# Optimization experiments

Measured on AMD Instinct MI355X. Metric: run time of the kernel, lower is better.

The kernel has to match this reference:

```python
import jax, jax.numpy as jnp
from jax import lax
import numpy as np

B, C_IN, IMG = 128, 3, 64
NH, D, K = 128, 256, 1024
BETA = 0.1        # beta buffer initialized to beta_start
BA_ITERS = 5
EPS = 1e-10


def _conv(x, w, b, stride, pad):
    y = lax.conv_general_dilated(x, w, (stride, stride), ((pad, pad), (pad, pad)),
                                 dimension_numbers=("NCHW", "OIHW", "NCHW"))
    return y + b[None, :, None, None]


def _convT(x, w, b):
    # PyTorch ConvTranspose2d(k=4, s=2, p=1); w: [Cin, Cout, 4, 4]
    wt = jnp.flip(w, (2, 3)).transpose(1, 0, 2, 3)  # -> [Cout, Cin, 4, 4]
    y = lax.conv_general_dilated(x, wt, (1, 1), ((2, 2), (2, 2)),
                                 lhs_dilation=(2, 2),
                                 dimension_numbers=("NCHW", "OIHW", "NCHW"))
    return y + b[None, :, None, None]


def _res(x, w1, b1, w2, b2):
    h = jax.nn.relu(_conv(x, w1, b1, 1, 1))
    h = _conv(h, w2, b2, 1, 1)
    return jax.nn.relu(h + x)


def setup_inputs() -> dict:
    key = jax.random.key(0)
    ks = iter(jax.random.split(key, 40))

    def w(shape):
        fan_in = int(np.prod(shape[1:]))
        return jax.random.normal(next(ks), shape, jnp.float32) / np.float32(np.sqrt(fan_in))

    z = lambda n: jnp.zeros((n,), jnp.float32)
    inp = {"x": jax.random.normal(next(ks), (B, C_IN, IMG, IMG), jnp.float32)}
    inp.update(
        ew1=w((NH, 3, 4, 4)), eb1=z(NH),
        ew2=w((2 * NH, NH, 4, 4)), eb2=z(2 * NH),
        ew3=w((D, 2 * NH, 3, 3)), eb3=z(D),
        er1aw=w((D, D, 3, 3)), er1ab=z(D), er1bw=w((D, D, 3, 3)), er1bb=z(D),
        er2aw=w((D, D, 3, 3)), er2ab=z(D), er2bw=w((D, D, 3, 3)), er2bb=z(D),
        codebook=jax.random.uniform(next(ks), (K, D), jnp.float32, -1.0 / K, 1.0 / K),
        pi=jnp.full((K,), 1.0 / K, jnp.float32),
        dr1aw=w((D, D, 3, 3)), dr1ab=z(D), dr1bw=w((D, D, 3, 3)), dr1bb=z(D),
        dr2aw=w((D, D, 3, 3)), dr2ab=z(D), dr2bw=w((D, D, 3, 3)), dr2bb=z(D),
        dw1=w((2 * NH, D, 3, 3)), db1=z(2 * NH),
        dwt2=w((2 * NH, NH, 4, 4)), dbt2=z(NH),
        dwt3=w((NH, 3, 4, 4)), dbt3=z(3),
    )
    return inp


def reference(x, ew1, eb1, ew2, eb2, ew3, eb3,
              er1aw, er1ab, er1bw, er1bb, er2aw, er2ab, er2bw, er2bb,
              codebook, pi,
              dr1aw, dr1ab, dr1bw, dr1bb, dr2aw, dr2ab, dr2bw, dr2bb,
              dw1, db1, dwt2, dbt2, dwt3, dbt3):
    # ---- encoder: [B,3,H,W] -> [B,D,H/4,W/4] ----
    h = jax.nn.relu(_conv(x, ew1, eb1, 2, 1))
    h = jax.nn.relu(_conv(h, ew2, eb2, 2, 1))
    h = jax.nn.relu(_conv(h, ew3, eb3, 1, 1))
    h = _res(h, er1aw, er1ab, er1bw, er1bb)
    z = _res(h, er2aw, er2ab, er2bw, er2bb)

    Bn, Dn, Hl, Wl = z.shape
    zf = z.transpose(0, 2, 3, 1).reshape(-1, Dn)  # [N, D]

    # squared euclidean distances [N, K]
    d = (jnp.sum(zf * zf, axis=1, keepdims=True)
         + jnp.sum(codebook * codebook, axis=1)
         - 2.0 * (zf @ codebook.T))

    # ---- Blahut-Arimoto iterations ----
    Q = pi
    for _ in range(BA_ITERS):
        logits = jnp.log(jnp.clip(Q, EPS)) - BETA * d  # [N, K]
        P = jax.nn.softmax(logits, axis=1)
        Q = jnp.clip(jnp.mean(P, axis=0), EPS)

    zq_soft = P @ codebook                              # [N, D]
    idx = jnp.argmax(P, axis=1)

    commit = 0.25 * jnp.mean((zf - lax.stop_gradient(zq_soft)) ** 2)
    cb_loss = jnp.mean((zq_soft - lax.stop_gradient(zf)) ** 2)
    ent = -jnp.sum(Q * jnp.log(jnp.clip(Q, EPS)))
    ent_loss = -0.01 * ent

    zq_hard = codebook[idx]
    zq = zq_soft + lax.stop_gradient(zq_hard - zq_soft)  # straight-through
    zq = zq.reshape(Bn, Hl, Wl, Dn).transpose(0, 3, 1, 2)

    # ---- decoder ----
    h = _res(zq, dr1aw, dr1ab, dr1bw, dr1bb)
    h = _res(h, dr2aw, dr2ab, dr2bw, dr2bb)
    h = jax.nn.relu(_conv(h, dw1, db1, 1, 1))
    h = jax.nn.relu(_convT(h, dwt2, dbt2))
    x_recon = _convT(h, dwt3, dbt3)
    return x_recon, commit, cb_loss, ent_loss
```

## Files before the change

kernel.cpp:

```cpp
#include <hip/hip_runtime.h>
#include <math.h>

#define NB   128
#define DC   256
#define SP   256
#define NROW 32768
#define KCB  1024
#define BETA_F 0.1f
#define EPSQ 1e-10f

typedef __attribute__((ext_vector_type(8))) short s16x8;
typedef __attribute__((ext_vector_type(4))) short s16x4;
typedef __attribute__((ext_vector_type(4))) float f32x4;

__device__ __forceinline__ short f2bf(float f) {
  unsigned u = __builtin_bit_cast(unsigned, f);
  unsigned r = (u + 0x7FFFu + ((u >> 16) & 1u)) >> 16;
  return (short)r;
}
__device__ __forceinline__ float bf2f(short s) {
  unsigned u = ((unsigned)(unsigned short)s) << 16;
  return __builtin_bit_cast(float, u);
}
__device__ __forceinline__ unsigned pack2(float a, float b) {
  return (unsigned)(unsigned short)f2bf(a) | ((unsigned)(unsigned short)f2bf(b) << 16);
}

__global__ void init0_kernel(short* __restrict__ zerob)
{
  if (threadIdx.x < 8) zerob[threadIdx.x] = 0;
}

__global__ void w3t10_kernel(
    const float* __restrict__ w0, const float* __restrict__ w1,
    const float* __restrict__ w2, const float* __restrict__ w3,
    const float* __restrict__ w4, const float* __restrict__ w5,
    const float* __restrict__ w6, const float* __restrict__ w7,
    const float* __restrict__ w8, const float* __restrict__ w9,
    short* __restrict__ o)
{
  const float* ws[10] = {w0, w1, w2, w3, w4, w5, w6, w7, w8, w9};
  const float* w = ws[blockIdx.y];
  const int i = blockIdx.x * 256 + threadIdx.x;
  const int ci = i & 255, co = (i >> 8) & 255, j = i >> 16;
  o[(size_t)blockIdx.y * 589824 + i] = f2bf(w[((size_t)(co * 256 + ci)) * 9 + j]);
}
__global__ void w2t_kernel(const float* __restrict__ w, short* __restrict__ o)
{
  const int i = blockIdx.x * 256 + threadIdx.x;
  const int ci = i & 127, co = (i >> 7) & 255, j = i >> 15;
  o[i] = f2bf(w[((size_t)(co * 128 + ci)) * 16 + j]);
}
__global__ void wtt2_kernel(const float* __restrict__ w, short* __restrict__ o)
{
  const int i = blockIdx.x * 256 + threadIdx.x;
  const int ci = i & 255, co = (i >> 8) & 127, j = (i >> 15) & 3, p = i >> 17;
  const int po = p >> 1, pq = p & 1, a = j >> 1, b2 = j & 1;
  const int kh = (1 - po) + 2 * a, kw = (1 - pq) + 2 * b2;
  o[i] = f2bf(w[((size_t)(ci * 128 + co)) * 16 + kh * 4 + kw]);
}
__global__ void cbbf_kernel(const float* __restrict__ cb, short* __restrict__ o)
{
  const int i = blockIdx.x * 256 + threadIdx.x;
  o[i] = f2bf(cb[i]);
}
__global__ void cbt_kernel(const float* __restrict__ cb, short* __restrict__ o)
{
  const int i = blockIdx.x * 256 + threadIdx.x;
  const int d = i >> 10, k = i & 1023;
  o[i] = f2bf(cb[(size_t)k * 256 + d]);
}

__global__ __launch_bounds__(256) void conv1_kernel(
    const float* __restrict__ x, const float* __restrict__ w,
    const float* __restrict__ bias, short* __restrict__ out)
{
  __shared__ float li[3][34][34];
  const int tid = threadIdx.x;
  const int tile = blockIdx.x;
  const int b = blockIdx.y;
  const int qy = tile >> 1, qx = tile & 1;
  const int ihlo = qy * 32 - 1, iwlo = qx * 32 - 1;
  for (int ci = 0; ci < 3; ++ci)
    for (int s = tid; s < 1156; s += 256) {
      const int r = s / 34, c = s - r * 34;
      const int ih = ihlo + r, iw = iwlo + c;
      float v = 0.f;
      if ((unsigned)ih < 64u && (unsigned)iw < 64u)
        v = x[((size_t)(b * 3 + ci) * 64 + ih) * 64 + iw];
      li[ci][r][c] = v;
    }
  __syncthreads();

  const int wv = tid >> 6, l = tid & 63;
  const int co0 = 2 * l, co1 = 2 * l + 1;
  float w0[48], w1[48];
#pragma unroll
  for (int j = 0; j < 48; ++j) {
    w0[j] = w[(size_t)co0 * 48 + j];
    w1[j] = w[(size_t)co1 * 48 + j];
  }
  const float b0 = bias[co0], b1 = bias[co1];

  for (int pass = 0; pass < 64; ++pass) {
    const int pix = pass * 4 + wv;
    const int py = pix >> 4, px = pix & 15;
    float s0 = b0, s1 = b1;
#pragma unroll
    for (int ci = 0; ci < 3; ++ci)
#pragma unroll
      for (int kh = 0; kh < 4; ++kh)
#pragma unroll
        for (int kw = 0; kw < 4; ++kw) {
          const int j = ci * 16 + kh * 4 + kw;
          const float v = li[ci][2 * py + kh][2 * px + kw];
          s0 = fmaf(v, w0[j], s0);
          s1 = fmaf(v, w1[j], s1);
        }
    s0 = fmaxf(s0, 0.f);
    s1 = fmaxf(s1, 0.f);
    const int oh = qy * 16 + py, ow = qx * 16 + px;
    ((unsigned*)(out + ((size_t)b * 1024 + oh * 32 + ow) * 128))[l] = pack2(s0, s1);
  }
}

template<int MODE, int KIT, int AK, int KPN, int TS>
__global__ __launch_bounds__(256) void igemm_kernel(
    const short* __restrict__ Abuf, const short* __restrict__ Bw,
    const float* __restrict__ bias, const short* __restrict__ res,
    short* __restrict__ outb, float* __restrict__ outf32,
    float* __restrict__ sacc, const short* __restrict__ zerob)
{
  __shared__ __align__(16) short Alds[3][8192];
  __shared__ float red[4];
  const int tid = threadIdx.x;
  const int wv = tid >> 6, l = tid & 63;
  const int wm = wv >> 1, wn = wv & 1;
  const int lcol = l & 15, lk = l >> 4;
  const int m0 = blockIdx.x * 128;

  int ncol0 = 0, po = 0, pq = 0;
  const short* Bp = Bw;
  if constexpr (MODE == 3) {
    po = blockIdx.y >> 1; pq = blockIdx.y & 1;
    Bp += (size_t)blockIdx.y * 131072;
  } else {
    ncol0 = blockIdx.y * 128;
    Bp += (size_t)ncol0 * KPN;
  }

  const int cpos = l & 3;
  const int rl_[2] = { (wv * 2) * 16 + (l >> 2), (wv * 2 + 1) * 16 + (l >> 2) };
  const int cc_[2] = { cpos ^ ((rl_[0] >> 1) & 3), cpos ^ ((rl_[1] >> 1) & 3) };

  f32x4 acc[4][4];
#pragma unroll
  for (int i = 0; i < 4; ++i)
#pragma unroll
    for (int j = 0; j < 4; ++j) acc[i][j] = (f32x4){0.f, 0.f, 0.f, 0.f};

  const int aoff_base = lcol * 32 + ((lk ^ ((lcol >> 1) & 3)) * 8);

  auto STAGE = [&](int it, int bufc) {
    int jj, kk;
    if constexpr (MODE == 0 || MODE == 3) { jj = it >> 3; kk = it & 7; }
    else if constexpr (MODE == 2)         { jj = it >> 2; kk = it & 3; }
    else                                  { jj = 0; kk = it; }
    const int choff = kk * 32;
    (void)jj;
#pragma unroll
    for (int q = 0; q < 2; ++q) {
      const int rl = rl_[q], cc = cc_[q];
      const int m = m0 + rl;
      const short* srcA;
      if constexpr (MODE == 0) {
        const int q3 = jj / 3;
        const int ih = ((m >> 4) & 15) + q3 - 1, iw = (m & 15) + (jj - q3 * 3) - 1;
        const bool v = ((unsigned)ih < 16u) & ((unsigned)iw < 16u);
        srcA = v ? Abuf + (size_t)((m & ~255) + ih * 16 + iw) * AK + choff + cc * 8 : zerob;
      } else if constexpr (MODE == 2) {
        const int ih = 2 * ((m >> 4) & 15) + (jj >> 2) - 1, iw = 2 * (m & 15) + (jj & 3) - 1;
        const bool v = ((unsigned)ih < 32u) & ((unsigned)iw < 32u);
        srcA = v ? Abuf + (size_t)((m >> 8) * 1024 + ih * 32 + iw) * AK + choff + cc * 8 : zerob;
      } else if constexpr (MODE == 3) {
        const int ih = ((m >> 4) & 15) + po - (jj >> 1), iw = (m & 15) + pq - (jj & 1);
        const bool v = ((unsigned)ih < 16u) & ((unsigned)iw < 16u);
        srcA = v ? Abuf + (size_t)((m & ~255) + ih * 16 + iw) * AK + choff + cc * 8 : zerob;
      } else {
        srcA = Abuf + (size_t)m * AK + choff + cc * 8;
      }
      __builtin_amdgcn_global_load_lds(
          (const __attribute__((address_space(1))) void*)srcA,
          (__attribute__((address_space(3))) void*)(&Alds[bufc][(wv * 2 + q) * 512]),
          16, 0, 0);
      const short* srcB = Bp + (size_t)jj * TS + (size_t)rl * KPN + choff + cc * 8;
      __builtin_amdgcn_global_load_lds(
          (const __attribute__((address_space(1))) void*)srcB,
          (__attribute__((address_space(3))) void*)(&Alds[bufc][4096 + (wv * 2 + q) * 512]),
          16, 0, 0);
    }
  };

  auto COMPUTE = [&](int bufc) {
    s16x8 a[4], b[4];
#pragma unroll
    for (int ms = 0; ms < 4; ++ms)
      a[ms] = *(const s16x8*)&Alds[bufc][wm * 2048 + ms * 512 + aoff_base];
#pragma unroll
    for (int ns = 0; ns < 4; ++ns)
      b[ns] = *(const s16x8*)&Alds[bufc][4096 + wn * 2048 + ns * 512 + aoff_base];
#pragma unroll
    for (int ms = 0; ms < 4; ++ms)
#pragma unroll
      for (int ns = 0; ns < 4; ++ns)
        acc[ms][ns] = __builtin_amdgcn_mfma_f32_16x16x32_bf16(a[ms], b[ns], acc[ms][ns], 0, 0, 0);
  };

  STAGE(0, 0);
  STAGE(1, 1);
  int buf = 0, nbuf = 2;
#pragma unroll 1
  for (int it = 0; it < KIT; ++it) {
    if (it + 1 < KIT) {
      asm volatile("s_waitcnt vmcnt(4)" ::: "memory");
    } else {
      asm volatile("s_waitcnt vmcnt(0)" ::: "memory");
    }
    __builtin_amdgcn_s_barrier();
    __builtin_amdgcn_sched_barrier(0);
    if (it + 2 < KIT) STAGE(it + 2, nbuf);
    __builtin_amdgcn_s_setprio(1);
    COMPUTE(buf);
    __builtin_amdgcn_s_setprio(0);
    buf = (buf == 2) ? 0 : buf + 1;
    nbuf = (nbuf == 2) ? 0 : nbuf + 1;
  }

  const int r4 = lk * 4;
  float ls = 0.f;
#pragma unroll
  for (int ms = 0; ms < 4; ++ms) {
#pragma unroll
    for (int ns = 0; ns < 4; ++ns) {
      const int n_l = wn * 64 + ns * 16 + lcol;
      const int n_g = ncol0 + n_l;
#pragma unroll
      for (int e = 0; e < 4; ++e) {
        const int m = m0 + wm * 64 + ms * 16 + r4 + e;
        if constexpr (MODE == 4) {
          const float val = bias[n_g] - 2.f * acc[ms][ns][e];
          outb[(size_t)m * 1024 + n_g] = f2bf(val);
        } else if constexpr (MODE == 5) {
          const float d = acc[ms][ns][e] - outf32[(size_t)m * 256 + n_g];
          ls = fmaf(d, d, ls);
        } else if constexpr (MODE == 3) {
          const float val = fmaxf(acc[ms][ns][e] + bias[n_l], 0.f);
          const int orow = (m & ~255) * 4 + (2 * ((m >> 4) & 15) + po) * 32 + (2 * (m & 15) + pq);
          outb[(size_t)orow * 128 + n_l] = f2bf(val);
        } else {
          float val = acc[ms][ns][e] + bias[n_g];
          if (res) val += bf2f(res[(size_t)m * 256 + n_g]);
          val = fmaxf(val, 0.f);
          outb[(size_t)m * 256 + n_g] = f2bf(val);
          if (outf32) outf32[(size_t)m * 256 + n_g] = val;
        }
      }
    }
  }
  if constexpr (MODE == 5) {
#pragma unroll
    for (int o = 32; o > 0; o >>= 1) ls += __shfl_xor(ls, o);
    if (l == 0) red[wv] = ls;
    __syncthreads();
    if (tid == 0) atomicAdd(sacc, red[0] + red[1] + red[2] + red[3]);
  }
}

__global__ __launch_bounds__(256) void rownorm_kernel(
    const float* __restrict__ a, float* __restrict__ nrm, int rows)
{
  const int wv = threadIdx.x >> 6, lane = threadIdx.x & 63;
  const int r = blockIdx.x * 4 + wv;
  if (r >= rows) return;
  const float* p = a + (size_t)r * DC;
  float s = 0.f;
#pragma unroll
  for (int i = 0; i < 4; ++i) { float v = p[lane + 64 * i]; s = fmaf(v, v, s); }
#pragma unroll
  for (int o = 32; o > 0; o >>= 1) s += __shfl_xor(s, o);
  if (lane == 0) nrm[r] = s;
}

__global__ void initq_kernel(const float* __restrict__ pi, float* __restrict__ logq,
                             float* __restrict__ Sacc)
{
  const int k = blockIdx.x * 256 + threadIdx.x;
  logq[k] = logf(fmaxf(pi[k], EPSQ));
  if (k == 0) *Sacc = 0.f;
}

__global__ __launch_bounds__(256) void ba2_kernel(
    uint4* __restrict__ DV, const float* __restrict__ logq,
    float* __restrict__ part, int* __restrict__ idxout, int storeP)
{
  __shared__ float qp[4][1024];
  const int tid = threadIdx.x;
  const int wv = tid >> 6, lane = tid & 63;

  float lq[16];
  {
    const float4* lq4 = (const float4*)logq;
#pragma unroll
    for (int h = 0; h < 2; ++h) {
      const float4 a = lq4[h * 128 + 2 * lane];
      const float4 b = lq4[h * 128 + 2 * lane + 1];
      lq[h * 8 + 0] = a.x; lq[h * 8 + 1] = a.y; lq[h * 8 + 2] = a.z; lq[h * 8 + 3] = a.w;
      lq[h * 8 + 4] = b.x; lq[h * 8 + 5] = b.y; lq[h * 8 + 6] = b.z; lq[h * 8 + 7] = b.w;
    }
  }

  float qacc[16];
#pragma unroll
  for (int j = 0; j < 16; ++j) qacc[j] = 0.f;

  const int n0 = blockIdx.x * 16;
  for (int rr = 0; rr < 4; ++rr) {
    const int n = n0 + wv * 4 + rr;
    uint4* rowp = DV + (size_t)n * 128;
    uint4 w[2];
    w[0] = rowp[lane];
    w[1] = rowp[64 + lane];
    float lv[16];
    float mx = -1e30f;
#pragma unroll
    for (int h = 0; h < 2; ++h) {
      const unsigned* u = (const unsigned*)&w[h];
#pragma unroll
      for (int p = 0; p < 4; ++p) {
        lv[h * 8 + 2 * p]     = lq[h * 8 + 2 * p]     - BETA_F * bf2f((short)(u[p] & 0xFFFFu));
        lv[h * 8 + 2 * p + 1] = lq[h * 8 + 2 * p + 1] - BETA_F * bf2f((short)(u[p] >> 16));
      }
    }
#pragma unroll
    for (int j = 0; j < 16; ++j) mx = fmaxf(mx, lv[j]);
#pragma unroll
    for (int o = 32; o > 0; o >>= 1) mx = fmaxf(mx, __shfl_xor(mx, o));
    float e[16];
    float s = 0.f;
#pragma unroll
    for (int j = 0; j < 16; ++j) { e[j] = __expf(lv[j] - mx); s += e[j]; }
#pragma unroll
    for (int o = 32; o > 0; o >>= 1) s += __shfl_xor(s, o);
    const float inv = 1.f / s;
#pragma unroll
    for (int j = 0; j < 16; ++j) qacc[j] += e[j] * inv;

    if (storeP) {
#pragma unroll
      for (int h = 0; h < 2; ++h) {
        unsigned* u = (unsigned*)&w[h];
#pragma unroll
        for (int p = 0; p < 4; ++p)
          u[p] = pack2(e[h * 8 + 2 * p] * inv, e[h * 8 + 2 * p + 1] * inv);
      }
      rowp[lane] = w[0];
      rowp[64 + lane] = w[1];
      float bv = lv[0]; int bi = 8 * lane;
#pragma unroll
      for (int h = 0; h < 2; ++h)
#pragma unroll
        for (int j = 0; j < 8; ++j) {
          const int k = h * 512 + 8 * lane + j;
          const float v = lv[h * 8 + j];
          if (v > bv || (v == bv && k < bi)) { bv = v; bi = k; }
        }
#pragma unroll
      for (int o = 32; o > 0; o >>= 1) {
        const float ov = __shfl_xor(bv, o);
        const int oi = __shfl_xor(bi, o);
        if (ov > bv || (ov == bv && oi < bi)) { bv = ov; bi = oi; }
      }
      if (lane == 0) idxout[n] = bi;
    }
  }
  __syncthreads();
#pragma unroll
  for (int h = 0; h < 2; ++h)
#pragma unroll
    for (int j = 0; j < 8; ++j)
      qp[wv][h * 512 + 8 * lane + j] = qacc[h * 8 + j];
  __syncthreads();
  for (int k = tid; k < 1024; k += 256) {
    part[(size_t)blockIdx.x * 1024 + k] = qp[0][k] + qp[1][k] + qp[2][k] + qp[3][k];
  }
}

__global__ __launch_bounds__(256) void qred1_kernel(
    const float* __restrict__ part, float* __restrict__ part2)
{
  const int b = blockIdx.x;
  const int tid = threadIdx.x;
  const float* p = part + (size_t)b * 32 * 1024;
#pragma unroll
  for (int j = 0; j < 4; ++j) {
    const int k = tid + j * 256;
    float s = 0.f;
#pragma unroll
    for (int r = 0; r < 32; ++r) s += p[(size_t)r * 1024 + k];
    part2[(size_t)b * 1024 + k] = s;
  }
}

__global__ __launch_bounds__(256) void qred2_kernel(
    const float* __restrict__ part2, float* __restrict__ qsum, float* __restrict__ logq)
{
  const int k = blockIdx.x * 256 + threadIdx.x;
  float s = 0.f;
#pragma unroll
  for (int r = 0; r < 64; ++r) s += part2[(size_t)r * 1024 + k];
  qsum[k] = s;
  logq[k] = logf(fmaxf(s * (1.f / 32768.f), EPSQ));
}

__global__ __launch_bounds__(1024) void ent_kernel(
    const float* __restrict__ qsum, float* __restrict__ out_ent)
{
  const int k = threadIdx.x;
  const float q = fmaxf(qsum[k] * (1.f / 32768.f), EPSQ);
  float v = q * logf(q);
#pragma unroll
  for (int o = 32; o > 0; o >>= 1) v += __shfl_xor(v, o);
  __shared__ float red[16];
  const int wv = k >> 6, lane = k & 63;
  if (lane == 0) red[wv] = v;
  __syncthreads();
  if (k == 0) {
    float s = 0.f;
    for (int i = 0; i < 16; ++i) s += red[i];
    *out_ent = 0.01f * s;
  }
}

__global__ void scalars_kernel(const float* __restrict__ S, float* __restrict__ out2)
{
  const float s = *S;
  out2[0] = 0.25f * s / 8388608.f;
  out2[1] = s / 8388608.f;
}

__global__ void gather16_kernel(const int* __restrict__ idx, const short* __restrict__ cbb,
                                short* __restrict__ out)
{
  const int t = blockIdx.x * 256 + threadIdx.x;
  const int m = t >> 6, d4 = (t & 63) * 4;
  *(s16x4*)(out + (size_t)m * 256 + d4) = *(const s16x4*)(cbb + (size_t)idx[m] * 256 + d4);
}

__global__ __launch_bounds__(256) void convt3_kernel(
    const short* __restrict__ in, const float* __restrict__ w,
    const float* __restrict__ bias, float* __restrict__ out)
{
  __shared__ __align__(16) short li[100 * 128];
  __shared__ float lw[6144];
  const int tid = threadIdx.x;
  const int tile = blockIdx.x;
  const int b = blockIdx.y;
  const int ty0 = (tile >> 2) * 16, tx0 = (tile & 3) * 16;
  const int iy0 = (tile >> 2) * 8 - 1, ix0 = (tile & 3) * 8 - 1;
  for (int s = tid; s < 1600; s += 256) {
    const int pix = s >> 4, ch = s & 15;
    const int r = pix / 10, c = pix - r * 10;
    const int ih = iy0 + r, iw = ix0 + c;
    s16x8 v = {0, 0, 0, 0, 0, 0, 0, 0};
    if ((unsigned)ih < 32u && (unsigned)iw < 32u)
      v = *(const s16x8*)(in + ((size_t)b * 1024 + ih * 32 + iw) * 128 + ch * 8);
    const int slot = ch ^ (pix & 15);
    *(s16x8*)&li[pix * 128 + slot * 8] = v;
  }
  for (int s = tid; s < 6144; s += 256) lw[s] = w[s];
  __syncthreads();
  const int ty = tid >> 4, tx = tid & 15;
  const int oh2 = ty0 + ty, ow2 = tx0 + tx;
  const int kh0 = (oh2 + 1) & 1, kw0 = (ow2 + 1) & 1;
  const int ih0 = (oh2 + 1 - kh0) >> 1, iw0 = (ow2 + 1 - kw0) >> 1;
  const int rl0 = ih0 - iy0, cl0 = iw0 - ix0;
  const int p00 = rl0 * 10 + cl0, p01 = p00 - 1, p10 = p00 - 10, p11 = p00 - 11;
  const int wi00 = kh0 * 4 + kw0, wi01 = wi00 + 2, wi10 = wi00 + 8, wi11 = wi00 + 10;
  float acc0 = 0.f, acc1 = 0.f, acc2 = 0.f;
  for (int ch = 0; ch < 16; ++ch) {
    const s16x8 v00 = *(const s16x8*)&li[p00 * 128 + (ch ^ (p00 & 15)) * 8];
    const s16x8 v01 = *(const s16x8*)&li[p01 * 128 + (ch ^ (p01 & 15)) * 8];
    const s16x8 v10 = *(const s16x8*)&li[p10 * 128 + (ch ^ (p10 & 15)) * 8];
    const s16x8 v11 = *(const s16x8*)&li[p11 * 128 + (ch ^ (p11 & 15)) * 8];
#pragma unroll
    for (int e = 0; e < 8; ++e) {
      const int ci = ch * 8 + e;
      const float* wr = &lw[ci * 48];
      const float f00 = bf2f(v00[e]), f01 = bf2f(v01[e]);
      const float f10 = bf2f(v10[e]), f11 = bf2f(v11[e]);
      acc0 = fmaf(wr[wi00], f00, fmaf(wr[wi01], f01, fmaf(wr[wi10], f10, fmaf(wr[wi11], f11, acc0))));
      acc1 = fmaf(wr[16 + wi00], f00, fmaf(wr[16 + wi01], f01, fmaf(wr[16 + wi10], f10, fmaf(wr[16 + wi11], f11, acc1))));
      acc2 = fmaf(wr[32 + wi00], f00, fmaf(wr[32 + wi01], f01, fmaf(wr[32 + wi10], f10, fmaf(wr[32 + wi11], f11, acc2))));
    }
  }
  const size_t ob = ((size_t)(b * 3) * 64 + oh2) * 64 + ow2;
  out[ob] = acc0 + bias[0];
  out[ob + 4096] = acc1 + bias[1];
  out[ob + 8192] = acc2 + bias[2];
}

extern "C" void kernel_launch(void* const* d_in, const int* in_sizes, int n_in,
                              void* d_out, int out_size, void* d_ws, size_t ws_size,
                              hipStream_t stream)
{
  const float* x     = (const float*)d_in[0];
  const float* ew1   = (const float*)d_in[1];
  const float* eb1   = (const float*)d_in[2];
  const float* ew2   = (const float*)d_in[3];
  const float* eb2   = (const float*)d_in[4];
  const float* ew3   = (const float*)d_in[5];
  const float* eb3   = (const float*)d_in[6];
  const float* er1aw = (const float*)d_in[7];
  const float* er1ab = (const float*)d_in[8];
  const float* er1bw = (const float*)d_in[9];
  const float* er1bb = (const float*)d_in[10];
  const float* er2aw = (const float*)d_in[11];
  const float* er2ab = (const float*)d_in[12];
  const float* er2bw = (const float*)d_in[13];
  const float* er2bb = (const float*)d_in[14];
  const float* cb    = (const float*)d_in[15];
  const float* pi    = (const float*)d_in[16];
  const float* dr1aw = (const float*)d_in[17];
  const float* dr1ab = (const float*)d_in[18];
  const float* dr1bw = (const float*)d_in[19];
  const float* dr1bb = (const float*)d_in[20];
  const float* dr2aw = (const float*)d_in[21];
  const float* dr2ab = (const float*)d_in[22];
  const float* dr2bw = (const float*)d_in[23];
  const float* dr2bb = (const float*)d_in[24];
  const float* dw1   = (const float*)d_in[25];
  const float* db1   = (const float*)d_in[26];
  const float* dwt2  = (const float*)d_in[27];
  const float* dbt2  = (const float*)d_in[28];
  const float* dwt3  = (const float*)d_in[29];
  const float* dbt3  = (const float*)d_in[30];

  float* outf = (float*)d_out;

  char* W = (char*)d_ws;
  short* BIGA  = (short*)W;
  float* ZF32  = (float*)W;
  short* DV    = (short*)(W + 33554432);
  short* X0    = (short*)(W + 100663296);
  short* X1    = (short*)(W + 117440512);
  short* X2    = (short*)(W + 134217728);
  short* WT2   = (short*)(W + 152174592);
  short* WTT2  = (short*)(W + 153223168);
  short* CBB   = (short*)(W + 154271744);
  short* CBT   = (short*)(W + 154796032);
  float* cn    = (float*)(W + 155320320);
  float* qsum  = (float*)(W + 155324416);
  float* logq  = (float*)(W + 155328512);
  int*   idx   = (int*)(W + 155332608);
  float* Sacc  = (float*)(W + 155463680);
  short* zerob = (short*)(W + 155463696);
  float* PART  = (float*)(W + 160000000);
  float* PART2 = (float*)(W + 168388608);
  short* WT3S  = (short*)(W + 168650752);

  const dim3 blk(256);
  #define WTSLAB(i) (WT3S + (size_t)(i) * 589824)
  #define IG3(A_, Wi_, B_, R_, O_, F_) \
    igemm_kernel<0,72,256,256,65536><<<dim3(256, 2), blk, 0, stream>>>( \
        A_, WTSLAB(Wi_), B_, R_, O_, F_, nullptr, zerob)

  init0_kernel<<<dim3(1), dim3(64), 0, stream>>>(zerob);
  w3t10_kernel<<<dim3(2304, 10), blk, 0, stream>>>(
      ew3, er1aw, er1bw, er2aw, er2bw, dr1aw, dr1bw, dr2aw, dr2bw, dw1, WT3S);

  conv1_kernel<<<dim3(4, NB), blk, 0, stream>>>(x, ew1, eb1, BIGA);
  w2t_kernel<<<dim3(2048), blk, 0, stream>>>(ew2, WT2);
  igemm_kernel<2,64,128,128,32768><<<dim3(256, 2), blk, 0, stream>>>(
      BIGA, WT2, eb2, nullptr, X0, nullptr, nullptr, zerob);
  IG3(X0, 0, eb3, nullptr, X1, nullptr);
  IG3(X1, 1, er1ab, nullptr, X2, nullptr);
  IG3(X2, 2, er1bb, X1, X0, nullptr);
  IG3(X0, 3, er2ab, nullptr, X1, nullptr);
  IG3(X1, 4, er2bb, X0, X2, ZF32);

  rownorm_kernel<<<dim3(KCB / 4), blk, 0, stream>>>(cb, cn, KCB);
  cbbf_kernel<<<dim3(1024), blk, 0, stream>>>(cb, CBB);
  cbt_kernel<<<dim3(1024), blk, 0, stream>>>(cb, CBT);
  initq_kernel<<<dim3(4), blk, 0, stream>>>(pi, logq, Sacc);
  igemm_kernel<4,8,256,256,0><<<dim3(256, 8), blk, 0, stream>>>(
      X2, CBB, cn, nullptr, DV, nullptr, nullptr, zerob);
  for (int i = 0; i < 5; ++i) {
    ba2_kernel<<<dim3(NROW / 16), blk, 0, stream>>>(
        (uint4*)DV, logq, PART, idx, (i == 4) ? 1 : 0);
    qred1_kernel<<<dim3(64), blk, 0, stream>>>(PART, PART2);
    qred2_kernel<<<dim3(4), blk, 0, stream>>>(PART2, qsum, logq);
  }
  ent_kernel<<<dim3(1), dim3(1024), 0, stream>>>(qsum, outf + 1572866);
  igemm_kernel<5,32,1024,1024,0><<<dim3(256, 2), blk, 0, stream>>>(
      DV, CBT, nullptr, nullptr, nullptr, ZF32, Sacc, zerob);
  scalars_kernel<<<dim3(1), dim3(1), 0, stream>>>(Sacc, outf + 1572864);
  gather16_kernel<<<dim3(8192), blk, 0, stream>>>(idx, CBB, X0);

  IG3(X0, 5, dr1ab, nullptr, X1, nullptr);
  IG3(X1, 6, dr1bb, X0, X2, nullptr);
  IG3(X2, 7, dr2ab, nullptr, X0, nullptr);
  IG3(X0, 8, dr2bb, X2, X1, nullptr);
  IG3(X1, 9, db1, nullptr, X0, nullptr);
  wtt2_kernel<<<dim3(2048), blk, 0, stream>>>(dwt2, WTT2);
  igemm_kernel<3,32,256,256,32768><<<dim3(256, 4), blk, 0, stream>>>(
      X0, WTT2, dbt2, nullptr, BIGA, nullptr, nullptr, zerob);
  convt3_kernel<<<dim3(16, NB), blk, 0, stream>>>(BIGA, dwt3, dbt3, outf);
  #undef IG3
  #undef WTSLAB
}
```

Measured before the change: 976.8 us.

## Deepen igemm prefetch to 4 stages, fuse Q reductions, merge scalar kernels

The implicit-GEMM main loop moves from a 3-buffer to a 4-buffer LDS ring with three tiles in flight, which hides more global-load latency at the cost of more LDS per block and possibly lower occupancy. The two-kernel Q reduction becomes one kernel in which the last-arriving block, found through an atomic ticket, does the final sum and log. The entropy and scalar-loss kernels are merged, cutting launch count in the Blahut-Arimoto loop. convt3 now converts its inputs to fp32 once when staging them into LDS instead of in the inner loop, which doubles that kernel's LDS footprint.

```diff
diff --git a/kernel.cpp b/kernel.cpp
--- a/kernel.cpp
+++ b/kernel.cpp
@@ -26,9 +26,10 @@
   return (unsigned)(unsigned short)f2bf(a) | ((unsigned)(unsigned short)f2bf(b) << 16);
 }
 
-__global__ void init0_kernel(short* __restrict__ zerob)
+__global__ void init0_kernel(short* __restrict__ zerob, unsigned* __restrict__ ticket)
 {
   if (threadIdx.x < 8) zerob[threadIdx.x] = 0;
+  if (threadIdx.x == 0) *ticket = 0u;
 }
 
 __global__ void w3t10_kernel(
@@ -131,7 +132,7 @@
     short* __restrict__ outb, float* __restrict__ outf32,
     float* __restrict__ sacc, const short* __restrict__ zerob)
 {
-  __shared__ __align__(16) short Alds[3][8192];
+  __shared__ __align__(16) short Alds[4][8192];
   __shared__ float red[4];
   const int tid = threadIdx.x;
   const int wv = tid >> 6, l = tid & 63;
@@ -218,22 +219,25 @@
 
   STAGE(0, 0);
   STAGE(1, 1);
-  int buf = 0, nbuf = 2;
+  STAGE(2, 2);
+  int buf = 0, nbuf = 3;
 #pragma unroll 1
   for (int it = 0; it < KIT; ++it) {
-    if (it + 1 < KIT) {
+    if (it + 2 < KIT) {
+      asm volatile("s_waitcnt vmcnt(8)" ::: "memory");
+    } else if (it + 1 < KIT) {
       asm volatile("s_waitcnt vmcnt(4)" ::: "memory");
     } else {
       asm volatile("s_waitcnt vmcnt(0)" ::: "memory");
     }
     __builtin_amdgcn_s_barrier();
     __builtin_amdgcn_sched_barrier(0);
-    if (it + 2 < KIT) STAGE(it + 2, nbuf);
+    if (it + 3 < KIT) STAGE(it + 3, nbuf);
     __builtin_amdgcn_s_setprio(1);
     COMPUTE(buf);
     __builtin_amdgcn_s_setprio(0);
-    buf = (buf == 2) ? 0 : buf + 1;
-    nbuf = (nbuf == 2) ? 0 : nbuf + 1;
+    buf = (buf + 1) & 3;
+    nbuf = (nbuf + 1) & 3;
   }
 
   const int r4 = lk * 4;
@@ -395,8 +399,9 @@
   }
 }
 
-__global__ __launch_bounds__(256) void qred1_kernel(
-    const float* __restrict__ part, float* __restrict__ part2)
+__global__ __launch_bounds__(256) void qredf_kernel(
+    const float* __restrict__ part, float* __restrict__ part2,
+    float* __restrict__ qsum, float* __restrict__ logq, unsigned* __restrict__ ticket)
 {
   const int b = blockIdx.x;
   const int tid = threadIdx.x;
@@ -409,21 +414,27 @@
     for (int r = 0; r < 32; ++r) s += p[(size_t)r * 1024 + k];
     part2[(size_t)b * 1024 + k] = s;
   }
-}
-
-__global__ __launch_bounds__(256) void qred2_kernel(
-    const float* __restrict__ part2, float* __restrict__ qsum, float* __restrict__ logq)
-{
-  const int k = blockIdx.x * 256 + threadIdx.x;
-  float s = 0.f;
-#pragma unroll
-  for (int r = 0; r < 64; ++r) s += part2[(size_t)r * 1024 + k];
-  qsum[k] = s;
-  logq[k] = logf(fmaxf(s * (1.f / 32768.f), EPSQ));
-}
-
-__global__ __launch_bounds__(1024) void ent_kernel(
-    const float* __restrict__ qsum, float* __restrict__ out_ent)
+  __threadfence();
+  __shared__ unsigned lastv;
+  if (tid == 0) lastv = atomicAdd(ticket, 1u);
+  __syncthreads();
+  if (lastv == 63u) {
+    __threadfence();
+#pragma unroll
+    for (int j = 0; j < 4; ++j) {
+      const int k = tid + j * 256;
+      float s = 0.f;
+#pragma unroll
+      for (int r = 0; r < 64; ++r) s += part2[(size_t)r * 1024 + k];
+      qsum[k] = s;
+      logq[k] = logf(fmaxf(s * (1.f / 32768.f), EPSQ));
+    }
+    if (tid == 0) *ticket = 0u;
+  }
+}
+
+__global__ __launch_bounds__(1024) void entsc_kernel(
+    const float* __restrict__ qsum, const float* __restrict__ S, float* __restrict__ out3)
 {
   const int k = threadIdx.x;
   const float q = fmaxf(qsum[k] * (1.f / 32768.f), EPSQ);
@@ -437,15 +448,11 @@
   if (k == 0) {
     float s = 0.f;
     for (int i = 0; i < 16; ++i) s += red[i];
-    *out_ent = 0.01f * s;
-  }
-}
-
-__global__ void scalars_kernel(const float* __restrict__ S, float* __restrict__ out2)
-{
-  const float s = *S;
-  out2[0] = 0.25f * s / 8388608.f;
-  out2[1] = s / 8388608.f;
+    out3[2] = 0.01f * s;
+    const float sa = *S;
+    out3[0] = 0.25f * sa / 8388608.f;
+    out3[1] = sa / 8388608.f;
+  }
 }
 
 __global__ void gather16_kernel(const int* __restrict__ idx, const short* __restrict__ cbb,
@@ -460,7 +467,7 @@
     const short* __restrict__ in, const float* __restrict__ w,
     const float* __restrict__ bias, float* __restrict__ out)
 {
-  __shared__ __align__(16) short li[100 * 128];
+  __shared__ __align__(16) float li[100 * 128];
   __shared__ float lw[6144];
   const int tid = threadIdx.x;
   const int tile = blockIdx.x;
@@ -475,7 +482,11 @@
     if ((unsigned)ih < 32u && (unsigned)iw < 32u)
       v = *(const s16x8*)(in + ((size_t)b * 1024 + ih * 32 + iw) * 128 + ch * 8);
     const int slot = ch ^ (pix & 15);
-    *(s16x8*)&li[pix * 128 + slot * 8] = v;
+    f32x4 f0, f1;
+#pragma unroll
+    for (int e = 0; e < 4; ++e) { f0[e] = bf2f(v[e]); f1[e] = bf2f(v[e + 4]); }
+    *(f32x4*)&li[pix * 128 + slot * 8] = f0;
+    *(f32x4*)&li[pix * 128 + slot * 8 + 4] = f1;
   }
   for (int s = tid; s < 6144; s += 256) lw[s] = w[s];
   __syncthreads();
@@ -488,19 +499,22 @@
   const int wi00 = kh0 * 4 + kw0, wi01 = wi00 + 2, wi10 = wi00 + 8, wi11 = wi00 + 10;
   float acc0 = 0.f, acc1 = 0.f, acc2 = 0.f;
   for (int ch = 0; ch < 16; ++ch) {
-    const s16x8 v00 = *(const s16x8*)&li[p00 * 128 + (ch ^ (p00 & 15)) * 8];
-    const s16x8 v01 = *(const s16x8*)&li[p01 * 128 + (ch ^ (p01 & 15)) * 8];
-    const s16x8 v10 = *(const s16x8*)&li[p10 * 128 + (ch ^ (p10 & 15)) * 8];
-    const s16x8 v11 = *(const s16x8*)&li[p11 * 128 + (ch ^ (p11 & 15)) * 8];
+    float f00[8], f01[8], f10[8], f11[8];
+    *(f32x4*)&f00[0] = *(const f32x4*)&li[p00 * 128 + (ch ^ (p00 & 15)) * 8];
+    *(f32x4*)&f00[4] = *(const f32x4*)&li[p00 * 128 + (ch ^ (p00 & 15)) * 8 + 4];
+    *(f32x4*)&f01[0] = *(const f32x4*)&li[p01 * 128 + (ch ^ (p01 & 15)) * 8];
+    *(f32x4*)&f01[4] = *(const f32x4*)&li[p01 * 128 + (ch ^ (p01 & 15)) * 8 + 4];
+    *(f32x4*)&f10[0] = *(const f32x4*)&li[p10 * 128 + (ch ^ (p10 & 15)) * 8];
+    *(f32x4*)&f10[4] = *(const f32x4*)&li[p10 * 128 + (ch ^ (p10 & 15)) * 8 + 4];
+    *(f32x4*)&f11[0] = *(const f32x4*)&li[p11 * 128 + (ch ^ (p11 & 15)) * 8];
+    *(f32x4*)&f11[4] = *(const f32x4*)&li[p11 * 128 + (ch ^ (p11 & 15)) * 8 + 4];
 #pragma unroll
     for (int e = 0; e < 8; ++e) {
       const int ci = ch * 8 + e;
       const float* wr = &lw[ci * 48];
-      const float f00 = bf2f(v00[e]), f01 = bf2f(v01[e]);
-      const float f10 = bf2f(v10[e]), f11 = bf2f(v11[e]);
-      acc0 = fmaf(wr[wi00], f00, fmaf(wr[wi01], f01, fmaf(wr[wi10], f10, fmaf(wr[wi11], f11, acc0))));
-      acc1 = fmaf(wr[16 + wi00], f00, fmaf(wr[16 + wi01], f01, fmaf(wr[16 + wi10], f10, fmaf(wr[16 + wi11], f11, acc1))));
-      acc2 = fmaf(wr[32 + wi00], f00, fmaf(wr[32 + wi01], f01, fmaf(wr[32 + wi10], f10, fmaf(wr[32 + wi11], f11, acc2))));
+      acc0 = fmaf(wr[wi00], f00[e], fmaf(wr[wi01], f01[e], fmaf(wr[wi10], f10[e], fmaf(wr[wi11], f11[e], acc0))));
+      acc1 = fmaf(wr[16 + wi00], f00[e], fmaf(wr[16 + wi01], f01[e], fmaf(wr[16 + wi10], f10[e], fmaf(wr[16 + wi11], f11[e], acc1))));
+      acc2 = fmaf(wr[32 + wi00], f00[e], fmaf(wr[32 + wi01], f01[e], fmaf(wr[32 + wi10], f10[e], fmaf(wr[32 + wi11], f11[e], acc2))));
     }
   }
   const size_t ob = ((size_t)(b * 3) * 64 + oh2) * 64 + ow2;
@@ -564,6 +578,7 @@
   int*   idx   = (int*)(W + 155332608);
   float* Sacc  = (float*)(W + 155463680);
   short* zerob = (short*)(W + 155463696);
+  unsigned* ticket = (unsigned*)(W + 155463712);
   float* PART  = (float*)(W + 160000000);
   float* PART2 = (float*)(W + 168388608);
   short* WT3S  = (short*)(W + 168650752);
@@ -574,7 +589,7 @@
     igemm_kernel<0,72,256,256,65536><<<dim3(256, 2), blk, 0, stream>>>( \
         A_, WTSLAB(Wi_), B_, R_, O_, F_, nullptr, zerob)
 
-  init0_kernel<<<dim3(1), dim3(64), 0, stream>>>(zerob);
+  init0_kernel<<<dim3(1), dim3(64), 0, stream>>>(zerob, ticket);
   w3t10_kernel<<<dim3(2304, 10), blk, 0, stream>>>(
       ew3, er1aw, er1bw, er2aw, er2bw, dr1aw, dr1bw, dr2aw, dr2bw, dw1, WT3S);
 
@@ -597,13 +612,11 @@
   for (int i = 0; i < 5; ++i) {
     ba2_kernel<<<dim3(NROW / 16), blk, 0, stream>>>(
         (uint4*)DV, logq, PART, idx, (i == 4) ? 1 : 0);
-    qred1_kernel<<<dim3(64), blk, 0, stream>>>(PART, PART2);
-    qred2_kernel<<<dim3(4), blk, 0, stream>>>(PART2, qsum, logq);
-  }
-  ent_kernel<<<dim3(1), dim3(1024), 0, stream>>>(qsum, outf + 1572866);
+    qredf_kernel<<<dim3(64), blk, 0, stream>>>(PART, PART2, qsum, logq, ticket);
+  }
   igemm_kernel<5,32,1024,1024,0><<<dim3(256, 2), blk, 0, stream>>>(
       DV, CBT, nullptr, nullptr, nullptr, ZF32, Sacc, zerob);
-  scalars_kernel<<<dim3(1), dim3(1), 0, stream>>>(Sacc, outf + 1572864);
+  entsc_kernel<<<dim3(1), dim3(1024), 0, stream>>>(qsum, Sacc, outf + 1572864);
   gather16_kernel<<<dim3(8192), blk, 0, stream>>>(idx, CBB, X0);
 
   IG3(X0, 5, dr1ab, nullptr, X1, nullptr);
```

Measured after the change: 965.9 us. No clear change (-1.1%).
